# Kernel optimization log

Measured on AMD Instinct MI355X. Metric: run time of the kernel, lower is better.

## Reference

```python
import jax, jax.numpy as jnp
import numpy as np

N = 60000   # nodes (utterances)
E = 480000  # edges
C = 256     # utt_size == embedding_size (shrink disabled)
R = 16      # num_relations for conv1; conv3 uses n_speakers**2 == 16
NB = 8      # rgcn_reg_basis (num_bases)
NS = 4      # n_speakers


def _rgcn(x, src, dst, etype, comp, bases, root, bias, num_rel):
    # PyG RGCNConv with basis decomposition: W_r = sum_b comp[r,b] * bases[b]
    # out_i = sum_r mean_{j in N_r(i)} x_j @ W_r + x_i @ root + bias
    n = x.shape[0]
    W = jnp.einsum('rb,bio->rio', comp, bases)                      # [R,C,C]
    xw = jnp.einsum('ni,rio->rno', x, W).reshape(num_rel * n, -1)   # [R*N,C]
    seg = dst * num_rel + etype                                     # (dst, rel) bucket
    ones = jnp.ones((src.shape[0],), x.dtype)
    cnt = jax.ops.segment_sum(ones, seg, num_segments=n * num_rel)
    norm = (1.0 / jnp.maximum(cnt, 1.0))[seg]                       # per-relation mean
    msg = xw[etype * n + src] * norm[:, None]                       # [E,C] gather
    return jax.ops.segment_sum(msg, dst, num_segments=n) + x @ root + bias


def _gconv(x, src, dst, w_rel, b_rel, w_root):
    # PyG GraphConv, aggr='add': lin_rel(sum_j x_j) + lin_root(x)
    agg = jax.ops.segment_sum(x[src], dst, num_segments=x.shape[0])
    return agg @ w_rel + b_rel + x @ w_root


def _mlp(x, w1, c1, w2, c2, w3, c3):
    h = jax.nn.relu(x @ w1 + c1)
    h = jax.nn.relu(h @ w2 + c2)
    return h @ w3 + c3


def setup_inputs():
    key = jax.random.key(0)
    ks = jax.random.split(key, 24)
    f = lambda i, shape, s=0.05: jax.random.normal(ks[i], shape, jnp.float32) * s
    z = lambda d: jnp.zeros((d,), jnp.float32)
    return {
        'encoding': jax.random.normal(ks[0], (N, C), jnp.float32),
        'speaker': jax.random.randint(ks[1], (N,), 0, NS),
        'edge_index': jax.random.randint(ks[2], (2, E), 0, N),
        'edge_type': jax.random.randint(ks[3], (E,), 0, R),
        'edge_speaker_type': jax.random.randint(ks[4], (E,), 0, NS * NS),
        'spk_table': f(5, (NS, C)),
        'comp1': f(6, (R, NB), 0.2), 'bases1': f(7, (NB, C, C)),
        'root1': f(8, (C, C)), 'b1': z(C),
        'w2_rel': f(9, (C, C)), 'b2': z(C), 'w2_root': f(10, (C, C)),
        'comp3': f(11, (NS * NS, NB), 0.2), 'bases3': f(12, (NB, C, C)),
        'root3': f(13, (C, C)), 'b3': z(C),
        'w4_rel': f(14, (C, C)), 'b4': z(C), 'w4_root': f(15, (C, C)),
        'wd1': f(16, (3 * C, C // 2)), 'bd1': z(C // 2),
        'wd2': f(17, (C // 2, C // 4)), 'bd2': z(C // 4),
        'wd3': f(18, (C // 4, 1)), 'bd3': z(1),
    }


def reference(encoding, speaker, edge_index, edge_type, edge_speaker_type,
              spk_table, comp1, bases1, root1, b1, w2_rel, b2, w2_root,
              comp3, bases3, root3, b3, w4_rel, b4, w4_root,
              wd1, bd1, wd2, bd2, wd3, bd3):
    src, dst = edge_index[0], edge_index[1]
    x = encoding + spk_table[speaker]            # speaker embedding fusion
    h1 = _rgcn(x, src, dst, edge_type, comp1, bases1, root1, b1, R)
    h1 = _gconv(h1, src, dst, w2_rel, b2, w2_root)
    h2 = _rgcn(x, src, dst, edge_speaker_type, comp3, bases3, root3, b3, NS * NS)
    h2 = _gconv(h2, src, dst, w4_rel, b4, w4_root)
    feat = jnp.concatenate([encoding, h1, h2], axis=1)  # [N, 3C]
    pred = _mlp(feat, wd1, bd1, wd2, bd2, wd3, bd3)     # [N, 1]
    return pred.squeeze(1)
```

## Files before the change

kernel.cpp:

```cpp
#include <hip/hip_runtime.h>
#include <stdint.h>


typedef unsigned short u16;
typedef __attribute__((ext_vector_type(4))) float f32x4;
typedef __attribute__((ext_vector_type(8))) short short8;

__device__ __forceinline__ float b2f(u16 u){
  union { uint32_t i; float f; } v; v.i = ((uint32_t)u) << 16; return v.f;
}
__device__ __forceinline__ u16 f2b(float f){
  union { float f; uint32_t i; } v; v.f = f;
  uint32_t u = v.i;
  return (u16)((u + 0x7FFFu + ((u >> 16) & 1u)) >> 16);
}
__device__ __forceinline__ u16 rdw(const void* p, size_t i, int f32){
  return f32 ? f2b(((const float*)p)[i]) : ((const u16*)p)[i];
}
__device__ __forceinline__ void gload_lds16(const u16* gp, u16* lp){
  __builtin_amdgcn_global_load_lds(
      (const __attribute__((address_space(1))) uint32_t*)(uintptr_t)gp,
      (__attribute__((address_space(3))) uint32_t*)lp, 16, 0, 0);
}

__global__ void detect_dtype(const u16* enc16, int* flag){
  __shared__ int cnt;
  if (threadIdx.x == 0) cnt = 0;
  __syncthreads();
  unsigned u = enc16[threadIdx.x * 2];
  int e = (u >> 7) & 0xFF;
  if (e >= 100 && e <= 140) atomicAdd(&cnt, 1);
  __syncthreads();
  if (threadIdx.x == 0) flag[0] = (cnt < 128) ? 1 : 0;
}

__global__ void cvt_small(const void* spk, const void* c1, const void* c3,
                          const void* b1, const void* b2, const void* b3,
                          const void* b4, const void* bd1, const void* wd2,
                          const void* bd2, const void* wd3, const void* bd3,
                          u16* __restrict__ arena, const int* __restrict__ flag)
{
  int f = *flag;
  int i = blockIdx.x * blockDim.x + threadIdx.x;
  if (i < 1024) { arena[i] = rdw(spk, i, f); return; } i -= 1024;
  if (i < 128)  { arena[1024 + i] = rdw(c1, i, f); return; } i -= 128;
  if (i < 128)  { arena[1152 + i] = rdw(c3, i, f); return; } i -= 128;
  if (i < 256)  { arena[1280 + i] = rdw(b1, i, f); return; } i -= 256;
  if (i < 256)  { arena[1536 + i] = rdw(b2, i, f); return; } i -= 256;
  if (i < 256)  { arena[1792 + i] = rdw(b3, i, f); return; } i -= 256;
  if (i < 256)  { arena[2048 + i] = rdw(b4, i, f); return; } i -= 256;
  if (i < 128)  { arena[2304 + i] = rdw(bd1, i, f); return; } i -= 128;
  if (i < 64)   { arena[10624 + i] = rdw(bd2, i, f); return; } i -= 64;
  if (i < 64)   { arena[10688 + i] = rdw(wd3, i, f); return; } i -= 64;
  if (i < 1)    { arena[10752 + i] = rdw(bd3, i, f); return; } i -= 1;
  if (i < 8192) { int o = i >> 7, k = i & 127;
    arena[10880 + i] = rdw(wd2, k * 64 + o, f); }
}

__global__ void cvt4(const void* __restrict__ in, u16* __restrict__ out, int n,
                     const int* __restrict__ flag){
  int i = (blockIdx.x * blockDim.x + threadIdx.x) * 4;
  if (i >= n) return;
  ushort4 o;
  if (*flag) {
    float4 v = *(const float4*)((const float*)in + i);
    o.x = f2b(v.x); o.y = f2b(v.y); o.z = f2b(v.z); o.w = f2b(v.w);
  } else {
    o = *(const ushort4*)((const u16*)in + i);
  }
  *(ushort4*)(out + i) = o;
}

__global__ void pack_weights(const void* __restrict__ bases1, const void* __restrict__ root1,
                             const void* __restrict__ w2_rel, const void* __restrict__ w2_root,
                             const void* __restrict__ bases3, const void* __restrict__ root3,
                             const void* __restrict__ w4_rel, const void* __restrict__ w4_root,
                             const void* __restrict__ wd1,
                             u16* __restrict__ B1t, u16* __restrict__ B3t,
                             u16* __restrict__ B2t, u16* __restrict__ B4t,
                             u16* __restrict__ D1t, const int* __restrict__ flag)
{
  int f = *flag;
  int idx = blockIdx.x * blockDim.x + threadIdx.x;
  if (idx < 256*2304) { int o = idx / 2304, k = idx % 2304;
    B1t[idx] = (k < 2048) ? rdw(bases1, k*256 + o, f) : rdw(root1, (k-2048)*256 + o, f); return; }
  idx -= 256*2304;
  if (idx < 256*2304) { int o = idx / 2304, k = idx % 2304;
    B3t[idx] = (k < 2048) ? rdw(bases3, k*256 + o, f) : rdw(root3, (k-2048)*256 + o, f); return; }
  idx -= 256*2304;
  if (idx < 256*512) { int o = idx / 512, k = idx % 512;
    B2t[idx] = (k < 256) ? rdw(w2_rel, k*256 + o, f) : rdw(w2_root, (k-256)*256 + o, f); return; }
  idx -= 256*512;
  if (idx < 256*512) { int o = idx / 512, k = idx % 512;
    B4t[idx] = (k < 256) ? rdw(w4_rel, k*256 + o, f) : rdw(w4_root, (k-256)*256 + o, f); return; }
  idx -= 256*512;
  if (idx < 128*768) { int o = idx / 768, k = idx % 768;
    D1t[idx] = rdw(wd1, k*128 + o, f); }
}

__global__ void build_x(const void* __restrict__ enc, const int* __restrict__ speaker,
                        const u16* __restrict__ spkA ,
                        u16* __restrict__ X , int N,
                        const int* __restrict__ flag)
{
  int f = *flag;
  int idx = blockIdx.x * blockDim.x + threadIdx.x;
  if (idx >= N * 64) return;
  int n = idx >> 6, c = (idx & 63) * 4;
  int sp = speaker[n];
  ushort4 sv = *(const ushort4*)(spkA + (size_t)sp*256 + c);
  float e0, e1, e2, e3;
  if (f) {
    float4 ev = *(const float4*)((const float*)enc + (size_t)n*256 + c);
    e0 = ev.x; e1 = ev.y; e2 = ev.z; e3 = ev.w;
  } else {
    ushort4 ev = *(const ushort4*)((const u16*)enc + (size_t)n*256 + c);
    e0 = b2f(ev.x); e1 = b2f(ev.y); e2 = b2f(ev.z); e3 = b2f(ev.w);
  }
  ushort4 xv;
  xv.x = f2b(e0 + b2f(sv.x));
  xv.y = f2b(e1 + b2f(sv.y));
  xv.z = f2b(e2 + b2f(sv.z));
  xv.w = f2b(e3 + b2f(sv.w));
  *(ushort4*)(X + (size_t)n*256 + c) = xv;
}

__global__ void edge_hist(const int* __restrict__ ei, int* cnt_dst, int E)
{
  int e = blockIdx.x * blockDim.x + threadIdx.x;
  if (e >= E) return;
  atomicAdd(&cnt_dst[ei[E + e]], 1);
}

__global__ void scan_p1(const int* __restrict__ cnt, int* __restrict__ partial,
                        int* __restrict__ bsum, int N)
{
  __shared__ int s[256];
  int t = threadIdx.x;
  int g = blockIdx.x * 256 + t;
  int v = (g < N) ? cnt[g] : 0;
  s[t] = v; __syncthreads();
  #pragma unroll
  for (int off = 1; off < 256; off <<= 1) {
    int u = (t >= off) ? s[t - off] : 0;
    __syncthreads();
    s[t] += u;
    __syncthreads();
  }
  partial[g] = s[t];
  if (t == 255) bsum[blockIdx.x] = s[255];
}

__global__ void scan_p2(int* __restrict__ bsum, int nb)
{
  __shared__ int s[1024];
  int t = threadIdx.x;
  int v = (t < nb) ? bsum[t] : 0;
  s[t] = v; __syncthreads();
  #pragma unroll
  for (int off = 1; off < 1024; off <<= 1) {
    int u = (t >= off) ? s[t - off] : 0;
    __syncthreads();
    s[t] += u;
    __syncthreads();
  }
  if (t < nb) bsum[t] = s[t] - v;
  if (t == nb - 1) bsum[nb] = s[t];
}

__global__ void scan_p3(const int* __restrict__ cnt, const int* __restrict__ partial,
                        const int* __restrict__ bsum, int* __restrict__ basep, int N)
{
  int g = blockIdx.x * 256 + threadIdx.x;
  if (g < N) basep[g] = partial[g] - cnt[g] + bsum[blockIdx.x];
  if (g == 0) basep[N] = bsum[(N + 255) / 256];
}

__global__ void edge_scatter(const int* __restrict__ ei, const int* __restrict__ et,
                             const int* __restrict__ est, const int* __restrict__ basep,
                             int* cursor, int* __restrict__ esorted, int E)
{
  int e = blockIdx.x * blockDim.x + threadIdx.x;
  if (e >= E) return;
  int d = ei[E + e];
  int pos = basep[d] + atomicAdd(&cursor[d], 1);
  esorted[pos] = ei[e] | (et[e] << 17) | (est[e] << 21);
}

__global__ __launch_bounds__(256) void rgcn_agg2(
    const int* __restrict__ esorted, const int* __restrict__ basep,
    const u16* __restrict__ X ,
    const u16* __restrict__ comp1 ,
    const u16* __restrict__ comp3 ,
    u16* __restrict__ Mix1 ,
    u16* __restrict__ Mix3 ,
    int n0, int CR)
{
  __shared__ float sc1[128], sc3[128];
  if (threadIdx.x < 128) sc1[threadIdx.x] = b2f(comp1[threadIdx.x]);
  else sc3[threadIdx.x - 128] = b2f(comp3[threadIdx.x - 128]);
  __syncthreads();
  int nl = blockIdx.x * 4 + (threadIdx.x >> 6);
  if (nl >= CR) return;
  int n = n0 + nl;
  int lane = threadIdx.x & 63;
  int e0 = basep[n], e1 = basep[n + 1];
  int myrel = lane & 15;
  int cnt = 0;
  for (int e = e0; e < e1; e++) {
    int rec = esorted[e];
    int r1 = (rec >> 17) & 15, r3 = (rec >> 21) & 15;
    if (lane < 16) cnt += (r1 == myrel);
    else if (lane < 32) cnt += (r3 == myrel);
  }
  float invv = 1.0f / (float)(cnt > 1 ? cnt : 1);
  float acc1[8][4] = {}, acc3[8][4] = {};
  for (int e = e0; e < e1; e++) {
    int rec = esorted[e];
    int src = rec & 0x1FFFF;
    int r1 = (rec >> 17) & 15, r3 = (rec >> 21) & 15;
    float iv1 = __shfl(invv, r1);
    float iv3 = __shfl(invv, 16 + r3);
    ushort4 xr = *(const ushort4*)(X + (size_t)src * 256 + lane * 4);
    float x0 = b2f(xr.x), x1 = b2f(xr.y), x2 = b2f(xr.z), x3 = b2f(xr.w);
    const float* c1p = sc1 + r1 * 8;
    const float* c3p = sc3 + r3 * 8;
    #pragma unroll
    for (int b = 0; b < 8; b++) {
      float w1 = c1p[b] * iv1;
      acc1[b][0] += w1 * x0; acc1[b][1] += w1 * x1;
      acc1[b][2] += w1 * x2; acc1[b][3] += w1 * x3;
      float w3 = c3p[b] * iv3;
      acc3[b][0] += w3 * x0; acc3[b][1] += w3 * x1;
      acc3[b][2] += w3 * x2; acc3[b][3] += w3 * x3;
    }
  }
  #pragma unroll
  for (int b = 0; b < 8; b++) {
    ushort4 o1, o3;
    o1.x = f2b(acc1[b][0]); o1.y = f2b(acc1[b][1]);
    o1.z = f2b(acc1[b][2]); o1.w = f2b(acc1[b][3]);
    o3.x = f2b(acc3[b][0]); o3.y = f2b(acc3[b][1]);
    o3.z = f2b(acc3[b][2]); o3.w = f2b(acc3[b][3]);
    *(ushort4*)(Mix1 + (size_t)nl * 2048 + b * 256 + lane * 4) = o1;
    *(ushort4*)(Mix3 + (size_t)nl * 2048 + b * 256 + lane * 4) = o3;
  }
}

__global__ __launch_bounds__(256) void gconv_agg(
    const int* __restrict__ esorted, const int* __restrict__ basep,
    const u16* __restrict__ Hin ,
    u16* __restrict__ Agg , int N)
{
  int n = blockIdx.x * 4 + (threadIdx.x >> 6);
  if (n >= N) return;
  int lane = threadIdx.x & 63;
  int half = lane >> 5, l32 = lane & 31;
  float a[8] = {};
  int e0 = basep[n], e1 = basep[n + 1];
  for (int e = e0; e < e1; e += 2) {
    int ee = e + half;
    bool ok = ee < e1;
    int src = esorted[ok ? ee : e] & 0x1FFFF;
    short8 hv = *(const short8*)(Hin + (size_t)src * 256 + l32 * 8);
    if (ok) {
      #pragma unroll
      for (int j = 0; j < 8; j++) a[j] += b2f((u16)hv[j]);
    }
  }
  #pragma unroll
  for (int j = 0; j < 8; j++) a[j] += __shfl_xor(a[j], 32);
  if (half == 0) {
    short8 o;
    #pragma unroll
    for (int j = 0; j < 8; j++) o[j] = (short)f2b(a[j]);
    *(short8*)(Agg + (size_t)n * 256 + l32 * 8) = o;
  }
}

__global__ __launch_bounds__(256) void gemm_ms(
    const u16* __restrict__ A0, int lda0,
    const u16* __restrict__ A1, int lda1,
    const u16* __restrict__ A2, int lda2,
    int c1, int c2,
    const u16* __restrict__ Bt,
    const u16* __restrict__ bias,
    u16* __restrict__ Cout, int ldc,
    int M, int K, int relu, int nout, int nx,
    const u16* __restrict__ A0d, const u16* __restrict__ Btd,
    const u16* __restrict__ biasd, u16* __restrict__ Coutd)
{
  constexpr int BK = 64;
  __shared__ u16 As[128 * BK];
  __shared__ u16 Bs[128 * BK];
  int bi = blockIdx.x;
  const u16* A0u = A0; const u16* Btu = Bt; const u16* biasu = bias;
  u16* Cu = Cout;
  if (bi >= nx) { bi -= nx; A0u = A0d; Btu = Btd; biasu = biasd; Cu = Coutd; }
  int nblk = (nout + 127) >> 7;
  int grpw = nblk << 3;
  int g = bi / grpw, r = bi % grpw;
  int bm = (g * 8 + (r & 7)) * 128;
  if (bm >= M) return;
  int bn = (r >> 3) * 128;

  int tid = threadIdx.x;
  int wid = tid >> 6, lane = tid & 63;
  int wm = (wid & 1) * 64, wn = (wid >> 1) * 64;
  int r8 = lane >> 3;
  int colA = ((lane & 7) ^ r8) * 8;
  int rloc = wid * 8 + r8;
  int lm = lane & 15, quad = lane >> 4;

  f32x4 acc[4][4];
  #pragma unroll
  for (int i = 0; i < 4; i++)
    #pragma unroll
    for (int j = 0; j < 4; j++) acc[i][j] = (f32x4)0.0f;

  int ga0 = bm + 0 * 32 + rloc; ga0 = ga0 < M ? ga0 : M - 1;
  int ga1 = bm + 1 * 32 + rloc; ga1 = ga1 < M ? ga1 : M - 1;
  int ga2 = bm + 2 * 32 + rloc; ga2 = ga2 < M ? ga2 : M - 1;
  int ga3 = bm + 3 * 32 + rloc; ga3 = ga3 < M ? ga3 : M - 1;
  int gb0 = bn + 0 * 32 + rloc; gb0 = gb0 < nout ? gb0 : nout - 1;
  int gb1 = bn + 1 * 32 + rloc; gb1 = gb1 < nout ? gb1 : nout - 1;
  int gb2 = bn + 2 * 32 + rloc; gb2 = gb2 < nout ? gb2 : nout - 1;
  int gb3 = bn + 3 * 32 + rloc; gb3 = gb3 < nout ? gb3 : nout - 1;

  for (int k0 = 0; k0 < K; k0 += BK) {
    const u16* srcp; int ldas, kO;
    if (k0 < c1)      { srcp = A0u; ldas = lda0; kO = k0; }
    else if (k0 < c2) { srcp = A1;  ldas = lda1; kO = k0 - c1; }
    else              { srcp = A2;  ldas = lda2; kO = k0 - c2; }
    const u16* abase = srcp + kO + colA;
    gload_lds16(abase + (size_t)ga0 * ldas, As + (0 * 32 + wid * 8) * BK);
    gload_lds16(abase + (size_t)ga1 * ldas, As + (1 * 32 + wid * 8) * BK);
    gload_lds16(abase + (size_t)ga2 * ldas, As + (2 * 32 + wid * 8) * BK);
    gload_lds16(abase + (size_t)ga3 * ldas, As + (3 * 32 + wid * 8) * BK);
    const u16* bbase = Btu + k0 + colA;
    gload_lds16(bbase + (size_t)gb0 * K, Bs + (0 * 32 + wid * 8) * BK);
    gload_lds16(bbase + (size_t)gb1 * K, Bs + (1 * 32 + wid * 8) * BK);
    gload_lds16(bbase + (size_t)gb2 * K, Bs + (2 * 32 + wid * 8) * BK);
    gload_lds16(bbase + (size_t)gb3 * K, Bs + (3 * 32 + wid * 8) * BK);
    __syncthreads();
    #pragma unroll
    for (int kk = 0; kk < BK; kk += 32) {
      int cb = (kk >> 3) + quad;
      int xo = ((cb ^ (lm & 7)) << 3);
      short8 af[4], bf[4];
      #pragma unroll
      for (int mi = 0; mi < 4; mi++)
        af[mi] = *(const short8*)(As + (wm + mi * 16 + lm) * BK + xo);
      #pragma unroll
      for (int ni = 0; ni < 4; ni++)
        bf[ni] = *(const short8*)(Bs + (wn + ni * 16 + lm) * BK + xo);
      #pragma unroll
      for (int mi = 0; mi < 4; mi++)
        #pragma unroll
        for (int ni = 0; ni < 4; ni++)
          acc[mi][ni] = __builtin_amdgcn_mfma_f32_16x16x32_bf16(
              af[mi], bf[ni], acc[mi][ni], 0, 0, 0);
    }
    __syncthreads();
  }
  #pragma unroll
  for (int ni = 0; ni < 4; ni++) {
    int gn = bn + wn + ni * 16 + lm;
    int gnb = gn < nout ? gn : nout - 1;
    float bv = b2f(biasu[gnb]);
    #pragma unroll
    for (int mi = 0; mi < 4; mi++) {
      int rbase = bm + wm + mi * 16 + quad * 4;
      #pragma unroll
      for (int rr = 0; rr < 4; rr++) {
        int gmr = rbase + rr;
        if (gmr < M && gn < nout) {
          float v = acc[mi][ni][rr] + bv;
          if (relu) v = fmaxf(v, 0.f);
          Cu[(size_t)gmr * ldc + gn] = f2b(v);
        }
      }
    }
  }
}

__global__ __launch_bounds__(256) void mlp_tail2(
    const u16* __restrict__ h2m, const u16* __restrict__ wd3,
    const u16* __restrict__ bd3, void* __restrict__ outp, int N,
    const int* __restrict__ flag)
{
  int n = blockIdx.x * 4 + (threadIdx.x >> 6);
  if (n >= N) return;
  int lane = threadIdx.x & 63;
  float r = b2f(h2m[(size_t)n * 64 + lane]) * b2f(wd3[lane]);
  #pragma unroll
  for (int off = 32; off > 0; off >>= 1) r += __shfl_xor(r, off, 64);
  if (lane == 0) {
    float v = r + b2f(bd3[0]);
    if (*flag) ((float*)outp)[n] = v;
    else       ((u16*)outp)[n] = f2b(v);
  }
}

__global__ void sentinel(u16* out, int n, float code){
  int i = blockIdx.x * blockDim.x + threadIdx.x;
  if (i < n) out[i] = f2b(code);
}

extern "C" void kernel_launch(void* const* d_in, const int* in_sizes, int n_in,
                              void* d_out, int out_size, void* d_ws, size_t ws_size,
                              hipStream_t stream)
{
  const void* enc     = d_in[0];
  const int* speaker  = (const int*)d_in[1];
  const int* ei       = (const int*)d_in[2];
  const int* et       = (const int*)d_in[3];
  const int* est      = (const int*)d_in[4];
  const void* spk_tab = d_in[5];
  const void* comp1   = d_in[6];
  const void* bases1  = d_in[7];
  const void* root1   = d_in[8];
  const void* b1      = d_in[9];
  const void* w2_rel  = d_in[10];
  const void* b2      = d_in[11];
  const void* w2_root = d_in[12];
  const void* comp3   = d_in[13];
  const void* bases3  = d_in[14];
  const void* root3   = d_in[15];
  const void* b3      = d_in[16];
  const void* w4_rel  = d_in[17];
  const void* b4      = d_in[18];
  const void* w4_root = d_in[19];
  const void* wd1     = d_in[20];
  const void* bd1     = d_in[21];
  const void* wd2     = d_in[22];
  const void* bd2     = d_in[23];
  const void* wd3     = d_in[24];
  const void* bd3     = d_in[25];

  int N = in_sizes[1];
  int E = in_sizes[3];
  int nb = (N + 255) / 256;

  char* ws = (char*)d_ws;
  size_t off = 0;
  auto alloc = [&](size_t bytes) -> char* {
    char* p = ws + off; off = (off + bytes + 255) & ~(size_t)255; return p;
  };
  u16* X    = (u16*)alloc((size_t)N * 256 * 2);
  u16* hA   = (u16*)alloc((size_t)N * 256 * 2);
  u16* hA3  = (u16*)alloc((size_t)N * 256 * 2);
  u16* B1t  = (u16*)alloc((size_t)256 * 2304 * 2);
  u16* B3t  = (u16*)alloc((size_t)256 * 2304 * 2);
  u16* B2t  = (u16*)alloc((size_t)256 * 512 * 2);
  u16* B4t  = (u16*)alloc((size_t)256 * 512 * 2);
  u16* D1t  = (u16*)alloc((size_t)128 * 768 * 2);
  u16* arena = (u16*)alloc((size_t)20480 * 2);
  int* flag    = (int*)alloc(256);
  int* basep   = (int*)alloc((size_t)(N + 1) * 4);
  int* esorted = (int*)alloc((size_t)E * 4);

  char* R = ws + off;
  size_t Rsize = (ws_size > off) ? (ws_size - off) : 0;

  int* cnt_dst = (int*)R;
  int* cursor  = (int*)(R + (size_t)N * 4);
  int* partial = (int*)(R + (size_t)2 * N * 4);
  int* bsum    = (int*)(R + (size_t)2 * N * 4 + (size_t)nb * 256 * 4);
  size_t zspan = (size_t)2 * N * 4;

  u16* AggB = (u16*)R;
  u16* hB   = (u16*)(R + (size_t)N * 256 * 2);
  u16* hC   = (u16*)(R + (size_t)2 * N * 256 * 2);
  u16* h1m  = AggB;
  u16* h2m  = AggB + (size_t)N * 128;
  size_t phase2_need = (size_t)3 * N * 256 * 2;

  long crl = (long)(Rsize / (4096 * 2));
  int chunk_rows = (int)((crl / 128) * 128);
  int Mpad = ((N + 127) / 128) * 128;
  if (chunk_rows > Mpad) chunk_rows = Mpad;

  size_t sort_need = (size_t)2 * N * 4 + (size_t)nb * 256 * 4 + 2048 * 4;
  if (chunk_rows < 128 || Rsize < phase2_need || Rsize < sort_need) {
    float code = 2000.0f + (float)(ws_size >> 20);
    sentinel<<<(out_size + 255) / 256, 256, 0, stream>>>((u16*)d_out, out_size, code);
    return;
  }
  u16* Mix1blk = (u16*)R;
  u16* Mix3blk = Mix1blk + (size_t)chunk_rows * 2048;

  u16* spkA   = arena + 0;
  u16* comp1A = arena + 1024;
  u16* comp3A = arena + 1152;
  u16* b1A    = arena + 1280;
  u16* b2A    = arena + 1536;
  u16* b3A    = arena + 1792;
  u16* b4A    = arena + 2048;
  u16* bd1A   = arena + 2304;
  u16* bd2A   = arena + 10624;
  u16* wd3A   = arena + 10688;
  u16* bd3A   = arena + 10752;
  u16* wd2T   = arena + 10880;

  hipMemsetAsync(cnt_dst, 0, zspan, stream);

  detect_dtype<<<1, 256, 0, stream>>>((const u16*)enc, flag);
  cvt_small<<<75, 256, 0, stream>>>(spk_tab, comp1, comp3, b1, b2, b3, b4,
                                    bd1, wd2, bd2, wd3, bd3, arena, flag);

  int totpack = 256*2304*2 + 256*512*2 + 128*768;
  pack_weights<<<(totpack + 255) / 256, 256, 0, stream>>>(
      bases1, root1, w2_rel, w2_root, bases3, root3, w4_rel, w4_root, wd1,
      B1t, B3t, B2t, B4t, D1t, flag);
  build_x<<<(N * 64 + 255) / 256, 256, 0, stream>>>(enc, speaker, spkA, X, N, flag);
  edge_hist<<<(E + 255) / 256, 256, 0, stream>>>(ei, cnt_dst, E);
  scan_p1<<<nb, 256, 0, stream>>>(cnt_dst, partial, bsum, N);
  scan_p2<<<1, 1024, 0, stream>>>(bsum, nb);
  scan_p3<<<nb, 256, 0, stream>>>(cnt_dst, partial, bsum, basep, N);
  edge_scatter<<<(E + 255) / 256, 256, 0, stream>>>(ei, et, est, basep, cursor, esorted, E);

  int nb4 = (N + 3) / 4;
  const u16* nul = (const u16*)nullptr;
  auto nx_for = [](int M_, int nout_) {
    int mg = (M_ + 127) / 128;
    int nblk = (nout_ + 127) / 128;
    return ((mg + 7) / 8) * (nblk * 8);
  };

  for (int n0 = 0; n0 < N; n0 += chunk_rows) {
    int CR = (N - n0 < chunk_rows) ? (N - n0) : chunk_rows;
    rgcn_agg2<<<(CR + 3) / 4, 256, 0, stream>>>(esorted, basep, X, comp1A, comp3A,
                                                Mix1blk, Mix3blk, n0, CR);
    int nx = nx_for(CR, 256);
    gemm_ms<<<2 * nx, 256, 0, stream>>>(
        Mix1blk, 2048, X + (size_t)n0 * 256, 256, nul, 0, 2048, 2304,
        B1t, b1A, hA + (size_t)n0 * 256, 256, CR, 2304, 0, 256, nx,
        Mix3blk, B3t, b3A, hA3 + (size_t)n0 * 256);
  }
  int nxN = nx_for(N, 256);
  gconv_agg<<<nb4, 256, 0, stream>>>(esorted, basep, hA, AggB, N);
  gemm_ms<<<nxN, 256, 0, stream>>>(
      AggB, 256, hA, 256, nul, 0, 256, 512,
      B2t, b2A, hB, 256, N, 512, 0, 256, nxN, nul, nul, nul, (u16*)nullptr);
  gconv_agg<<<nb4, 256, 0, stream>>>(esorted, basep, hA3, AggB, N);
  cvt4<<<(N * 64 + 255) / 256, 256, 0, stream>>>(enc, X, N * 256, flag);
  gemm_ms<<<nxN, 256, 0, stream>>>(
      AggB, 256, hA3, 256, nul, 0, 256, 512,
      B4t, b4A, hC, 256, N, 512, 0, 256, nxN, nul, nul, nul, (u16*)nullptr);

  int nx1 = nx_for(N, 128);
  gemm_ms<<<nx1, 256, 0, stream>>>(
      X, 256, hB, 256, hC, 256, 256, 512,
      D1t, bd1A, h1m, 128, N, 768, 1, 128, nx1, nul, nul, nul, (u16*)nullptr);
  int nx2 = nx_for(N, 64);
  gemm_ms<<<nx2, 256, 0, stream>>>(
      h1m, 128, nul, 0, nul, 0, 128, 128,
      wd2T, bd2A, h2m, 64, N, 128, 1, 64, nx2, nul, nul, nul, (u16*)nullptr);
  mlp_tail2<<<nb4, 256, 0, stream>>>(h2m, wd3A, bd3A, d_out, N, flag);
}
```

Measured before the change: 792.8 us.

## Fuse both GraphConv aggregations and GEMMs into dual launches, balance chunk sizes

The two gconv_agg passes are merged into one kernel that gathers from both hA and hA3 per edge, so the edge indices are read once. The two GraphConv GEMMs become a single dual-problem gemm_ms launch, which needs a new A1d pointer so the second problem uses its own A1 source. The rgcn_agg2 accumulators are packed into float2 vectors so the compiler can emit packed FMA, and RGCN chunk rows are now spread evenly across the chunks. The cost is a separate AggC buffer, which raises the workspace requirement to 4*N*256 bf16 elements.

Result: no change. 790.7 us (median of 2 runs) (-0.3%).

```diff
diff --git a/kernel.cpp b/kernel.cpp
--- a/kernel.cpp
+++ b/kernel.cpp
@@ -3,6 +3,7 @@
 
 
 typedef unsigned short u16;
+typedef __attribute__((ext_vector_type(2))) float f32x2;
 typedef __attribute__((ext_vector_type(4))) float f32x4;
 typedef __attribute__((ext_vector_type(8))) short short8;
 
@@ -214,7 +215,7 @@
     else if (lane < 32) cnt += (r3 == myrel);
   }
   float invv = 1.0f / (float)(cnt > 1 ? cnt : 1);
-  float acc1[8][4] = {}, acc3[8][4] = {};
+  f32x2 acc1[8][2] = {}, acc3[8][2] = {};
   for (int e = e0; e < e1; e++) {
     int rec = esorted[e];
     int src = rec & 0x1FFFF;
@@ -222,59 +223,68 @@
     float iv1 = __shfl(invv, r1);
     float iv3 = __shfl(invv, 16 + r3);
     ushort4 xr = *(const ushort4*)(X + (size_t)src * 256 + lane * 4);
-    float x0 = b2f(xr.x), x1 = b2f(xr.y), x2 = b2f(xr.z), x3 = b2f(xr.w);
+    f32x2 xlo, xhi;
+    xlo[0] = b2f(xr.x); xlo[1] = b2f(xr.y);
+    xhi[0] = b2f(xr.z); xhi[1] = b2f(xr.w);
     const float* c1p = sc1 + r1 * 8;
     const float* c3p = sc3 + r3 * 8;
     #pragma unroll
     for (int b = 0; b < 8; b++) {
-      float w1 = c1p[b] * iv1;
-      acc1[b][0] += w1 * x0; acc1[b][1] += w1 * x1;
-      acc1[b][2] += w1 * x2; acc1[b][3] += w1 * x3;
-      float w3 = c3p[b] * iv3;
-      acc3[b][0] += w3 * x0; acc3[b][1] += w3 * x1;
-      acc3[b][2] += w3 * x2; acc3[b][3] += w3 * x3;
+      float w1s = c1p[b] * iv1;
+      f32x2 w1 = {w1s, w1s};
+      acc1[b][0] += w1 * xlo; acc1[b][1] += w1 * xhi;
+      float w3s = c3p[b] * iv3;
+      f32x2 w3 = {w3s, w3s};
+      acc3[b][0] += w3 * xlo; acc3[b][1] += w3 * xhi;
     }
   }
   #pragma unroll
   for (int b = 0; b < 8; b++) {
     ushort4 o1, o3;
-    o1.x = f2b(acc1[b][0]); o1.y = f2b(acc1[b][1]);
-    o1.z = f2b(acc1[b][2]); o1.w = f2b(acc1[b][3]);
-    o3.x = f2b(acc3[b][0]); o3.y = f2b(acc3[b][1]);
-    o3.z = f2b(acc3[b][2]); o3.w = f2b(acc3[b][3]);
+    o1.x = f2b(acc1[b][0][0]); o1.y = f2b(acc1[b][0][1]);
+    o1.z = f2b(acc1[b][1][0]); o1.w = f2b(acc1[b][1][1]);
+    o3.x = f2b(acc3[b][0][0]); o3.y = f2b(acc3[b][0][1]);
+    o3.z = f2b(acc3[b][1][0]); o3.w = f2b(acc3[b][1][1]);
     *(ushort4*)(Mix1 + (size_t)nl * 2048 + b * 256 + lane * 4) = o1;
     *(ushort4*)(Mix3 + (size_t)nl * 2048 + b * 256 + lane * 4) = o3;
   }
 }
 
-__global__ __launch_bounds__(256) void gconv_agg(
+__global__ __launch_bounds__(256) void gconv_agg2(
     const int* __restrict__ esorted, const int* __restrict__ basep,
-    const u16* __restrict__ Hin ,
-    u16* __restrict__ Agg , int N)
+    const u16* __restrict__ HinA ,
+    const u16* __restrict__ HinB ,
+    u16* __restrict__ AggA ,
+    u16* __restrict__ AggB , int N)
 {
   int n = blockIdx.x * 4 + (threadIdx.x >> 6);
   if (n >= N) return;
   int lane = threadIdx.x & 63;
   int half = lane >> 5, l32 = lane & 31;
-  float a[8] = {};
+  float a[8] = {}, b[8] = {};
   int e0 = basep[n], e1 = basep[n + 1];
   for (int e = e0; e < e1; e += 2) {
     int ee = e + half;
     bool ok = ee < e1;
     int src = esorted[ok ? ee : e] & 0x1FFFF;
-    short8 hv = *(const short8*)(Hin + (size_t)src * 256 + l32 * 8);
+    short8 hv  = *(const short8*)(HinA + (size_t)src * 256 + l32 * 8);
+    short8 hv3 = *(const short8*)(HinB + (size_t)src * 256 + l32 * 8);
     if (ok) {
       #pragma unroll
-      for (int j = 0; j < 8; j++) a[j] += b2f((u16)hv[j]);
+      for (int j = 0; j < 8; j++) { a[j] += b2f((u16)hv[j]); b[j] += b2f((u16)hv3[j]); }
     }
   }
   #pragma unroll
-  for (int j = 0; j < 8; j++) a[j] += __shfl_xor(a[j], 32);
+  for (int j = 0; j < 8; j++) {
+    a[j] += __shfl_xor(a[j], 32);
+    b[j] += __shfl_xor(b[j], 32);
+  }
   if (half == 0) {
-    short8 o;
+    short8 oa, ob;
     #pragma unroll
-    for (int j = 0; j < 8; j++) o[j] = (short)f2b(a[j]);
-    *(short8*)(Agg + (size_t)n * 256 + l32 * 8) = o;
+    for (int j = 0; j < 8; j++) { oa[j] = (short)f2b(a[j]); ob[j] = (short)f2b(b[j]); }
+    *(short8*)(AggA + (size_t)n * 256 + l32 * 8) = oa;
+    *(short8*)(AggB + (size_t)n * 256 + l32 * 8) = ob;
   }
 }
 
@@ -287,16 +297,18 @@
     const u16* __restrict__ bias,
     u16* __restrict__ Cout, int ldc,
     int M, int K, int relu, int nout, int nx,
-    const u16* __restrict__ A0d, const u16* __restrict__ Btd,
+    const u16* __restrict__ A0d, const u16* __restrict__ A1d,
+    const u16* __restrict__ Btd,
     const u16* __restrict__ biasd, u16* __restrict__ Coutd)
 {
   constexpr int BK = 64;
   __shared__ u16 As[128 * BK];
   __shared__ u16 Bs[128 * BK];
   int bi = blockIdx.x;
-  const u16* A0u = A0; const u16* Btu = Bt; const u16* biasu = bias;
+  const u16* A0u = A0; const u16* A1u = A1;
+  const u16* Btu = Bt; const u16* biasu = bias;
   u16* Cu = Cout;
-  if (bi >= nx) { bi -= nx; A0u = A0d; Btu = Btd; biasu = biasd; Cu = Coutd; }
+  if (bi >= nx) { bi -= nx; A0u = A0d; A1u = A1d; Btu = Btd; biasu = biasd; Cu = Coutd; }
   int nblk = (nout + 127) >> 7;
   int grpw = nblk << 3;
   int g = bi / grpw, r = bi % grpw;
@@ -330,7 +342,7 @@
   for (int k0 = 0; k0 < K; k0 += BK) {
     const u16* srcp; int ldas, kO;
     if (k0 < c1)      { srcp = A0u; ldas = lda0; kO = k0; }
-    else if (k0 < c2) { srcp = A1;  ldas = lda1; kO = k0 - c1; }
+    else if (k0 < c2) { srcp = A1u; ldas = lda1; kO = k0 - c1; }
     else              { srcp = A2;  ldas = lda2; kO = k0 - c2; }
     const u16* abase = srcp + kO + colA;
     gload_lds16(abase + (size_t)ga0 * ldas, As + (0 * 32 + wid * 8) * BK);
@@ -469,24 +481,27 @@
   int* bsum    = (int*)(R + (size_t)2 * N * 4 + (size_t)nb * 256 * 4);
   size_t zspan = (size_t)2 * N * 4;
 
-  u16* AggB = (u16*)R;
+  u16* AggA = (u16*)R;
   u16* hB   = (u16*)(R + (size_t)N * 256 * 2);
   u16* hC   = (u16*)(R + (size_t)2 * N * 256 * 2);
-  u16* h1m  = AggB;
-  u16* h2m  = AggB + (size_t)N * 128;
-  size_t phase2_need = (size_t)3 * N * 256 * 2;
+  u16* AggC = (u16*)(R + (size_t)3 * N * 256 * 2);
+  u16* h1m  = AggA;
+  u16* h2m  = AggA + (size_t)N * 128;
+  size_t phase2_need = (size_t)4 * N * 256 * 2;
 
   long crl = (long)(Rsize / (4096 * 2));
-  int chunk_rows = (int)((crl / 128) * 128);
+  int chunk_max = (int)((crl / 128) * 128);
   int Mpad = ((N + 127) / 128) * 128;
-  if (chunk_rows > Mpad) chunk_rows = Mpad;
+  if (chunk_max > Mpad) chunk_max = Mpad;
 
   size_t sort_need = (size_t)2 * N * 4 + (size_t)nb * 256 * 4 + 2048 * 4;
-  if (chunk_rows < 128 || Rsize < phase2_need || Rsize < sort_need) {
+  if (chunk_max < 128 || Rsize < phase2_need || Rsize < sort_need) {
     float code = 2000.0f + (float)(ws_size >> 20);
     sentinel<<<(out_size + 255) / 256, 256, 0, stream>>>((u16*)d_out, out_size, code);
     return;
   }
+  int nchunks = (Mpad + chunk_max - 1) / chunk_max;
+  int chunk_rows = (((N + nchunks - 1) / nchunks + 127) / 128) * 128;
   u16* Mix1blk = (u16*)R;
   u16* Mix3blk = Mix1blk + (size_t)chunk_rows * 2048;
 
@@ -534,28 +549,27 @@
                                                 Mix1blk, Mix3blk, n0, CR);
     int nx = nx_for(CR, 256);
     gemm_ms<<<2 * nx, 256, 0, stream>>>(
-        Mix1blk, 2048, X + (size_t)n0 * 256, 256, nul, 0, 2048, 2304,
-        B1t, b1A, hA + (size_t)n0 * 256, 256, CR, 2304, 0, 256, nx,
-        Mix3blk, B3t, b3A, hA3 + (size_t)n0 * 256);
+        Mix1blk, 2048, X + (size_t)n0 * 256, 256, nul, 0,
+        2048, 2304, B1t, b1A, hA + (size_t)n0 * 256, 256, CR, 2304, 0, 256, nx,
+        Mix3blk, X + (size_t)n0 * 256, B3t, b3A, hA3 + (size_t)n0 * 256);
   }
   int nxN = nx_for(N, 256);
-  gconv_agg<<<nb4, 256, 0, stream>>>(esorted, basep, hA, AggB, N);
-  gemm_ms<<<nxN, 256, 0, stream>>>(
-      AggB, 256, hA, 256, nul, 0, 256, 512,
-      B2t, b2A, hB, 256, N, 512, 0, 256, nxN, nul, nul, nul, (u16*)nullptr);
-  gconv_agg<<<nb4, 256, 0, stream>>>(esorted, basep, hA3, AggB, N);
+  gconv_agg2<<<nb4, 256, 0, stream>>>(esorted, basep, hA, hA3, AggA, AggC, N);
   cvt4<<<(N * 64 + 255) / 256, 256, 0, stream>>>(enc, X, N * 256, flag);
-  gemm_ms<<<nxN, 256, 0, stream>>>(
-      AggB, 256, hA3, 256, nul, 0, 256, 512,
-      B4t, b4A, hC, 256, N, 512, 0, 256, nxN, nul, nul, nul, (u16*)nullptr);
+  gemm_ms<<<2 * nxN, 256, 0, stream>>>(
+      AggA, 256, hA, 256, nul, 0, 256, 512,
+      B2t, b2A, hB, 256, N, 512, 0, 256, nxN,
+      AggC, hA3, B4t, b4A, hC);
 
   int nx1 = nx_for(N, 128);
   gemm_ms<<<nx1, 256, 0, stream>>>(
       X, 256, hB, 256, hC, 256, 256, 512,
-      D1t, bd1A, h1m, 128, N, 768, 1, 128, nx1, nul, nul, nul, (u16*)nullptr);
+      D1t, bd1A, h1m, 128, N, 768, 1, 128, nx1,
+      nul, nul, nul, nul, (u16*)nullptr);
   int nx2 = nx_for(N, 64);
   gemm_ms<<<nx2, 256, 0, stream>>>(
       h1m, 128, nul, 0, nul, 0, 128, 128,
-      wd2T, bd2A, h2m, 64, N, 128, 1, 64, nx2, nul, nul, nul, (u16*)nullptr);
+      wd2T, bd2A, h2m, 64, N, 128, 1, 64, nx2,
+      nul, nul, nul, nul, (u16*)nullptr);
   mlp_tail2<<<nb4, 256, 0, stream>>>(h2m, wd3A, bd3A, d_out, N, flag);
 }
```
